# Kernel tuning notes

Hardware: AMD Instinct MI355X
Metric: run time of the kernel (lower is better)

## Reference

```python
import jax, jax.numpy as jnp
import numpy as np

N_EMBD = 1024
N_HEADS = 16
HEAD_DIM = N_EMBD // N_HEADS


def setup_inputs() -> dict:
    key = jax.random.key(0)
    ks = jax.random.split(key, 6)
    s = 1.0 / np.sqrt(N_EMBD)
    x = jax.random.normal(ks[0], (2, 2048, N_EMBD), dtype=jnp.float32)
    # torch Linear weights are [out, in]; y = x @ W.T
    Wk = jax.random.uniform(ks[1], (N_EMBD, N_EMBD), jnp.float32, -s, s)
    Wq = jax.random.uniform(ks[2], (N_EMBD, N_EMBD), jnp.float32, -s, s)
    Wv = jax.random.uniform(ks[3], (N_EMBD, N_EMBD), jnp.float32, -s, s)
    Wp = jax.random.uniform(ks[4], (N_EMBD, N_EMBD), jnp.float32, -s, s)
    bp = jax.random.uniform(ks[5], (N_EMBD,), jnp.float32, -s, s)
    return {"x": x, "Wq": Wq, "Wk": Wk, "Wv": Wv, "Wp": Wp, "bp": bp}


def reference(x, Wq, Wk, Wv, Wp, bp):
    B, T, C = x.shape
    H, D = N_HEADS, HEAD_DIM
    # projections (torch Linear: x @ W.T), reshape to [B, H, T, D]
    q = (x @ Wq.T).reshape(B, T, H, D).transpose(0, 2, 1, 3)
    k = (x @ Wk.T).reshape(B, T, H, D).transpose(0, 2, 1, 3)
    v = (x @ Wv.T).reshape(B, T, H, D).transpose(0, 2, 1, 3)
    # scaled causal attention, full [B,H,T,T] scores (faithful to original)
    att = jnp.einsum('bhqd,bhkd->bhqk', q, k) * (D ** -0.5)
    causal = jnp.tril(jnp.ones((T, T), dtype=bool))
    att = jnp.where(causal[None, None], att, -jnp.inf)
    att = jax.nn.softmax(att, axis=-1)
    out = jnp.einsum('bhqk,bhkd->bhqd', att, v)
    out = out.transpose(0, 2, 1, 3).reshape(B, T, C)
    return out @ Wp.T + bp
```

## Files before the change

kernel.cpp:

```cpp
#include <hip/hip_runtime.h>

typedef __bf16 bf16;
typedef __bf16 bf16x8 __attribute__((ext_vector_type(8)));
typedef float f32x4 __attribute__((ext_vector_type(4)));

#define DEV __device__ __forceinline__
#define NEG_BIG (-1.0e30f)


DEV bf16x8 load8(const bf16* p) { bf16x8 v; __builtin_memcpy(&v, p, 16); return v; }
DEV void store8(bf16* p, bf16x8 v) { __builtin_memcpy(p, &v, 16); }

DEV int sniff_bf16(const unsigned short* __restrict__ xr) {
  const int lane = threadIdx.x & 63;
  const unsigned short w = xr[lane * 2];
  const int e = (w >> 7) & 0xFF;
  const bool sane = ((w & 0x7FFF) == 0) || (e >= 97 && e <= 157);
  return __popcll(__ballot(sane)) >= 48;
}

DEV size_t frag_off(int row, int k) {
  const int rt = row >> 7, ks = k >> 6;
  const int chunk = (((row >> 4) & 7) * 2 + ((k >> 5) & 1)) * 64 + ((k >> 3) & 3) * 16 + (row & 15);
  return ((((size_t)rt * 16 + (size_t)ks) * 1024 + (size_t)chunk) << 3) | (size_t)(k & 7);
}

struct ConvArgs {
  const void* src[6];
  bf16* dst[6];
};

DEV bf16x8 cvt_load(const void* s, size_t e, int isbf) {
  bf16x8 v;
  if (isbf) v = load8((const bf16*)s + e);
  else {
    float tmp[8];
    __builtin_memcpy(tmp, (const float*)s + e, 32);
#pragma unroll
    for (int j = 0; j < 8; ++j) v[j] = (bf16)tmp[j];
  }
  return v;
}

__global__ __launch_bounds__(256) void convert_kernel(ConvArgs a) {
  const int isbf = sniff_bf16((const unsigned short*)a.src[0]);
  const int L = blockIdx.x;
  const int t = threadIdx.x;
  if (L == 1024) {
    if (t < 128) store8(a.dst[5] + t * 8, cvt_load(a.src[5], (size_t)t * 8, isbf));
    return;
  }
  int sel, tile;
  if (L < 512) { sel = 0; tile = L; }
  else         { sel = 1 + ((L - 512) >> 7); tile = (L - 512) & 127; }
  const int rt = tile >> 4, ks = tile & 15;
  const void* s = a.src[sel];
  bf16* d = a.dst[sel];

  __shared__ alignas(16) bf16 lds[128 * 9 * 8];
#pragma unroll
  for (int q = 0; q < 4; ++q) {
    const int lin = q * 256 + t;
    const int row = lin >> 3, k8 = lin & 7;
    const size_t se = (((size_t)(rt * 128 + row)) << 10) + (size_t)(ks * 64 + k8 * 8);
    store8(lds + (row * 9 + k8) * 8, cvt_load(s, se, isbf));
  }
  __syncthreads();
#pragma unroll
  for (int q = 0; q < 4; ++q) {
    const int c = q * 256 + t;
    const int row = ((c >> 7) & 7) * 16 + (c & 15);
    const int k8 = ((c >> 6) & 1) * 4 + ((c >> 4) & 3);
    store8(d + ((((size_t)tile << 10) + (size_t)c) << 3), load8(lds + (row * 9 + k8) * 8));
  }
}

DEV void gemm_reg_128(const bf16* __restrict__ A, const bf16* __restrict__ W,
                      int mblk, int nblk, f32x4 (&acc)[4][4]) {
  const int lane = threadIdx.x & 63, wid = threadIdx.x >> 6;
  const int wm = (wid >> 1) << 6, wn = (wid & 1) << 6;
  const int lr = lane & 15, lg = lane >> 4;
  const int arow = mblk * 128 + wm + lr;
  const int brow = nblk * 128 + wn + lr;

  const f32x4 zero = {0.f, 0.f, 0.f, 0.f};
#pragma unroll
  for (int i = 0; i < 4; ++i)
#pragma unroll
    for (int j = 0; j < 4; ++j) acc[i][j] = zero;

  for (int ks = 0; ks < 16; ++ks) {
    bf16x8 af[2][4], bf[2][4];
#pragma unroll
    for (int kh = 0; kh < 2; ++kh) {
      const int k = ks * 64 + kh * 32 + lg * 8;
#pragma unroll
      for (int i = 0; i < 4; ++i) af[kh][i] = load8(A + frag_off(arow + i * 16, k));
#pragma unroll
      for (int j = 0; j < 4; ++j) bf[kh][j] = load8(W + frag_off(brow + j * 16, k));
    }
#pragma unroll
    for (int kh = 0; kh < 2; ++kh)
#pragma unroll
      for (int i = 0; i < 4; ++i)
#pragma unroll
        for (int j = 0; j < 4; ++j)
          acc[i][j] = __builtin_amdgcn_mfma_f32_16x16x32_bf16(af[kh][i], bf[kh][j], acc[i][j], 0, 0, 0);
  }
}

DEV size_t frag_idx(int row, int col) {
  return ((size_t)(((col >> 5) * 4 + ((row >> 4) & 3)) * 64 + ((col >> 3) & 3) * 16 + (row & 15)) << 3)
         | (size_t)(col & 7);
}

__global__ __launch_bounds__(256, 3) void qkv_proj_kernel(
    const bf16* __restrict__ x, const bf16* __restrict__ Wq,
    const bf16* __restrict__ Wk, const bf16* __restrict__ Wv,
    bf16* __restrict__ q_ws, bf16* __restrict__ k_ws, bf16* __restrict__ vt_ws) {
  const int L = blockIdx.x;
  const int xcd = L & 7;
  const int idx = L >> 3;
  const int mblk = (xcd & 3) * 8 + (idx & 7);
  const int nm = (xcd >> 2) * 12 + (idx >> 3);
  const int nblk = nm & 7;
  const int mode = nm >> 3;
  const bf16* W = (mode == 0) ? Wq : (mode == 1) ? Wk : Wv;
  f32x4 acc[4][4];
  gemm_reg_128(x, W, mblk, nblk, acc);

  const int lane = threadIdx.x & 63, wid = threadIdx.x >> 6;
  const int wm = (wid >> 1) << 6, wn = (wid & 1) << 6;
  const int lr = lane & 15, lg = lane >> 4;
  const int m0 = mblk << 7, n0 = nblk << 7;
  const float vscale = (mode == 0) ? 0.125f : 1.0f;
  bf16* out = (mode == 0) ? q_ws : (mode == 1) ? k_ws : vt_ws;
#pragma unroll
  for (int i = 0; i < 4; ++i) {
#pragma unroll
    for (int r = 0; r < 4; ++r) {
      const int m = m0 + wm + i * 16 + lg * 4 + r;
      const int b = m >> 11, t = m & 2047;
#pragma unroll
      for (int j = 0; j < 4; ++j) {
        const int n = n0 + wn + j * 16 + lr;
        const int h = n >> 6, d = n & 63;
        const float v = acc[i][j][r] * vscale;
        const size_t base = ((size_t)(b * 16 + h) << 17) + ((size_t)(t >> 6) << 12);
        const size_t idx2 = base + ((mode < 2) ? frag_idx(t & 63, d) : frag_idx(d, t & 63));
        out[idx2] = (bf16)v;
      }
    }
  }
}

__global__ __launch_bounds__(128, 1) void attn_kernel(
    const bf16* __restrict__ q_ws, const bf16* __restrict__ k_ws,
    const bf16* __restrict__ vt_ws, bf16* __restrict__ a_ws) {
  const int L = blockIdx.x;
  const int xcd = L & 7;
  const int bh = xcd * 4 + ((L >> 3) & 3);
  const int p = L >> 5;
  const int tid = threadIdx.x;
  const int lane = tid & 63, w = tid >> 6;
  const int lr = lane & 15, lg = lane >> 4;
  const int fo = lg * 16 + lr;

  __shared__ alignas(16) bf16 Ps[2][32 * 72];
  bf16* ps = &Ps[w][0];

  const size_t hb = (size_t)bh << 17;
  const int b = bh >> 4, h = bh & 15;
  const f32x4 zero = {0.f, 0.f, 0.f, 0.f};

  for (int ph = 0; ph < 2; ++ph) {
    const int s = ph ? (63 - (p * 2 + w)) : (p * 2 + w);
    const int kmax = s >> 1;
    const size_t qtb = hb + ((size_t)(s >> 1) << 12);

    bf16x8 aq[2][2];
#pragma unroll
    for (int g = 0; g < 2; ++g) {
      const int rg = (s & 1) * 2 + g;
#pragma unroll
      for (int c2 = 0; c2 < 2; ++c2)
        aq[g][c2] = load8(q_ws + qtb + (size_t)(((c2 * 4 + rg) * 64 + fo) << 3));
    }

    f32x4 o_acc[2][4];
#pragma unroll
    for (int g = 0; g < 2; ++g)
#pragma unroll
      for (int j = 0; j < 4; ++j) o_acc[g][j] = zero;
    float lsum[2][4] = {{0.f, 0.f, 0.f, 0.f}, {0.f, 0.f, 0.f, 0.f}};

    auto load_k = [&](bf16x8 (&bk)[4][2], int kt) {
      const size_t ktb = hb + ((size_t)kt << 12);
#pragma unroll
      for (int j = 0; j < 4; ++j)
#pragma unroll
        for (int c2 = 0; c2 < 2; ++c2)
          bk[j][c2] = load8(k_ws + ktb + (size_t)(((c2 * 4 + j) * 64 + fo) << 3));
    };

    auto step = [&](const bf16x8 (&bk)[4][2], int kt, bool diag) {
      const size_t ktb = hb + ((size_t)kt << 12);
      bf16x8 bv[4][2];
#pragma unroll
      for (int j = 0; j < 4; ++j)
#pragma unroll
        for (int c2 = 0; c2 < 2; ++c2)
          bv[j][c2] = load8(vt_ws + ktb + (size_t)(((c2 * 4 + j) * 64 + fo) << 3));

      f32x4 sc[2][4];
#pragma unroll
      for (int g = 0; g < 2; ++g)
#pragma unroll
        for (int j = 0; j < 4; ++j) {
          sc[g][j] = __builtin_amdgcn_mfma_f32_16x16x32_bf16(aq[g][0], bk[j][0], zero, 0, 0, 0);
          sc[g][j] = __builtin_amdgcn_mfma_f32_16x16x32_bf16(aq[g][1], bk[j][1], sc[g][j], 0, 0, 0);
        }
      float pp[2][4][4];
#pragma unroll
      for (int g = 0; g < 2; ++g) {
#pragma unroll
        for (int j = 0; j < 4; ++j) {
#pragma unroll
          for (int r = 0; r < 4; ++r) {
            float v = sc[g][j][r];
            if (diag) {
              const int trow = s * 32 + g * 16 + lg * 4 + r;
              const int tcol = kt * 64 + j * 16 + lr;
              if (tcol > trow) v = NEG_BIG;
            }
            pp[g][j][r] = __expf(v);
          }
        }
#pragma unroll
        for (int r = 0; r < 4; ++r)
          lsum[g][r] += (pp[g][0][r] + pp[g][1][r]) + (pp[g][2][r] + pp[g][3][r]);
      }
#pragma unroll
      for (int g = 0; g < 2; ++g)
#pragma unroll
        for (int j = 0; j < 4; ++j)
#pragma unroll
          for (int r = 0; r < 4; ++r)
            ps[(g * 16 + lg * 4 + r) * 72 + j * 16 + lr] = (bf16)pp[g][j][r];
#pragma unroll
      for (int c2 = 0; c2 < 2; ++c2) {
#pragma unroll
        for (int g = 0; g < 2; ++g) {
          const bf16x8 ap = load8(ps + (g * 16 + lr) * 72 + c2 * 32 + lg * 8);
#pragma unroll
          for (int j = 0; j < 4; ++j)
            o_acc[g][j] = __builtin_amdgcn_mfma_f32_16x16x32_bf16(ap, bv[j][c2], o_acc[g][j], 0, 0, 0);
        }
      }
    };

    bf16x8 bkA[4][2], bkB[4][2];
    load_k(bkA, 0);
    int kt = 0;
    while (true) {
      if (kt < kmax) load_k(bkB, kt + 1);
      step(bkA, kt, kt == kmax);
      if (kt >= kmax) break;
      ++kt;
      if (kt < kmax) load_k(bkA, kt + 1);
      step(bkB, kt, kt == kmax);
      if (kt >= kmax) break;
      ++kt;
    }

#pragma unroll
    for (int g = 0; g < 2; ++g) {
#pragma unroll
      for (int r = 0; r < 4; ++r) {
        float v = lsum[g][r];
#pragma unroll
        for (int off = 1; off < 16; off <<= 1) v += __shfl_xor(v, off, 64);
        const float inv = 1.f / v;
        const int mrow = b * 2048 + s * 32 + g * 16 + lg * 4 + r;
#pragma unroll
        for (int j = 0; j < 4; ++j) {
          const int col = h * 64 + j * 16 + lr;
          a_ws[frag_off(mrow, col)] = (bf16)(o_acc[g][j][r] * inv);
        }
      }
    }
  }
}

__global__ __launch_bounds__(256, 3) void out_proj_kernel(
    const bf16* __restrict__ A, const bf16* __restrict__ Wp,
    const bf16* __restrict__ bp, void* __restrict__ out,
    const unsigned short* __restrict__ xraw) {
  const int L = blockIdx.x;
  const int xcd = L & 7;
  const int i2 = L >> 3;
  const int mblk = xcd * 4 + (i2 & 3);
  const int nblk = i2 >> 2;
  f32x4 acc[4][4];
  gemm_reg_128(A, Wp, mblk, nblk, acc);

  const int lane = threadIdx.x & 63, wid = threadIdx.x >> 6;
  const int wm = (wid >> 1) << 6, wn = (wid & 1) << 6;
  const int lr = lane & 15, lg = lane >> 4;
  const int m0 = mblk << 7, n0 = nblk << 7;
  const int isbf = sniff_bf16(xraw);
#pragma unroll
  for (int i = 0; i < 4; ++i) {
#pragma unroll
    for (int r = 0; r < 4; ++r) {
      const int m = m0 + wm + i * 16 + lg * 4 + r;
#pragma unroll
      for (int j = 0; j < 4; ++j) {
        const int n = n0 + wn + j * 16 + lr;
        const float v = acc[i][j][r] + (float)bp[n];
        const size_t idx = ((size_t)m << 10) | (size_t)n;
        if (isbf) ((bf16*)out)[idx] = (bf16)v;
        else      ((float*)out)[idx] = v;
      }
    }
  }
}

extern "C" void kernel_launch(void* const* d_in, const int* in_sizes, int n_in,
                              void* d_out, int out_size, void* d_ws, size_t ws_size,
                              hipStream_t stream) {
  (void)in_sizes; (void)n_in; (void)out_size;
  if (ws_size < (50u << 20)) return;

  char* ws = (char*)d_ws;
  bf16* q_ws  = (bf16*)(ws);
  bf16* k_ws  = (bf16*)(ws + (8u << 20));
  bf16* vt_ws = (bf16*)(ws + (16u << 20));
  bf16* a_ws  = (bf16*)(ws + (24u << 20));
  bf16* xc    = (bf16*)(ws + (32u << 20));
  bf16* Wqc   = (bf16*)(ws + (40u << 20));
  bf16* Wkc   = (bf16*)(ws + (42u << 20));
  bf16* Wvc   = (bf16*)(ws + (44u << 20));
  bf16* Wpc   = (bf16*)(ws + (46u << 20));
  bf16* bpc   = (bf16*)(ws + (48u << 20));

  ConvArgs ca;
  ca.src[0] = d_in[0]; ca.dst[0] = xc;
  ca.src[1] = d_in[1]; ca.dst[1] = Wqc;
  ca.src[2] = d_in[2]; ca.dst[2] = Wkc;
  ca.src[3] = d_in[3]; ca.dst[3] = Wvc;
  ca.src[4] = d_in[4]; ca.dst[4] = Wpc;
  ca.src[5] = d_in[5]; ca.dst[5] = bpc;
  convert_kernel<<<1025, 256, 0, stream>>>(ca);

  qkv_proj_kernel<<<768, 256, 0, stream>>>(xc, Wqc, Wkc, Wvc, q_ws, k_ws, vt_ws);
  attn_kernel<<<512, 128, 0, stream>>>(q_ws, k_ws, vt_ws, a_ws);
  out_proj_kernel<<<256, 256, 0, stream>>>(a_ws, Wpc, bpc, d_out,
                                           (const unsigned short*)d_in[0]);
}
```

Measured before the change: 209.0 us.

## Split attention into single-wave blocks per query strip and halve out-proj tiles

The attention kernel now runs one 64-thread wave per 32-row query strip, giving 2048 blocks instead of 512 blocks that each processed two strips over two phases. Strips are launched in longest-first order, and the diagonal key tile is processed first. The output projection switches to a direct-load 128x64 tile GEMM with 512 blocks instead of 128x128 tiles. The aim is better load balance and occupancy across CUs, in exchange for less operand reuse per block and more global loads.

```diff
diff --git a/kernel.cpp b/kernel.cpp
--- a/kernel.cpp
+++ b/kernel.cpp
@@ -154,139 +154,136 @@
   }
 }
 
-__global__ __launch_bounds__(128, 1) void attn_kernel(
+__global__ __launch_bounds__(64, 2) void attn_kernel(
     const bf16* __restrict__ q_ws, const bf16* __restrict__ k_ws,
     const bf16* __restrict__ vt_ws, bf16* __restrict__ a_ws) {
   const int L = blockIdx.x;
   const int xcd = L & 7;
-  const int bh = xcd * 4 + ((L >> 3) & 3);
-  const int p = L >> 5;
-  const int tid = threadIdx.x;
-  const int lane = tid & 63, w = tid >> 6;
+  const int idx = L >> 3;
+  const int bh = xcd * 4 + (idx & 3);
+  const int s = 63 - (idx >> 2);
+  const int qt = s >> 1;
+  const int rh = s & 1;
+  const int lane = threadIdx.x & 63;
   const int lr = lane & 15, lg = lane >> 4;
   const int fo = lg * 16 + lr;
 
-  __shared__ alignas(16) bf16 Ps[2][32 * 72];
-  bf16* ps = &Ps[w][0];
+  __shared__ alignas(16) bf16 Ps[32 * 72];
 
   const size_t hb = (size_t)bh << 17;
   const int b = bh >> 4, h = bh & 15;
   const f32x4 zero = {0.f, 0.f, 0.f, 0.f};
-
-  for (int ph = 0; ph < 2; ++ph) {
-    const int s = ph ? (63 - (p * 2 + w)) : (p * 2 + w);
-    const int kmax = s >> 1;
-    const size_t qtb = hb + ((size_t)(s >> 1) << 12);
-
-    bf16x8 aq[2][2];
+  const size_t qtb = hb + ((size_t)qt << 12);
+
+  bf16x8 aq[2][2];
+#pragma unroll
+  for (int g = 0; g < 2; ++g) {
+    const int rg = rh * 2 + g;
+#pragma unroll
+    for (int c2 = 0; c2 < 2; ++c2)
+      aq[g][c2] = load8(q_ws + qtb + (size_t)(((c2 * 4 + rg) * 64 + fo) << 3));
+  }
+
+  f32x4 o_acc[2][4];
+#pragma unroll
+  for (int g = 0; g < 2; ++g)
+#pragma unroll
+    for (int j = 0; j < 4; ++j) o_acc[g][j] = zero;
+  float lsum[2][4] = {{0.f, 0.f, 0.f, 0.f}, {0.f, 0.f, 0.f, 0.f}};
+
+  auto load_k = [&](bf16x8 (&bk)[4][2], int kt) {
+    const size_t ktb = hb + ((size_t)kt << 12);
+#pragma unroll
+    for (int j = 0; j < 4; ++j)
+#pragma unroll
+      for (int c2 = 0; c2 < 2; ++c2)
+        bk[j][c2] = load8(k_ws + ktb + (size_t)(((c2 * 4 + j) * 64 + fo) << 3));
+  };
+
+  auto step = [&](const bf16x8 (&bk)[4][2], int kt, bool diag) {
+    const size_t ktb = hb + ((size_t)kt << 12);
+    bf16x8 bv[4][2];
+#pragma unroll
+    for (int j = 0; j < 4; ++j)
+#pragma unroll
+      for (int c2 = 0; c2 < 2; ++c2)
+        bv[j][c2] = load8(vt_ws + ktb + (size_t)(((c2 * 4 + j) * 64 + fo) << 3));
+
+    f32x4 sc[2][4];
+#pragma unroll
+    for (int g = 0; g < 2; ++g)
+#pragma unroll
+      for (int j = 0; j < 4; ++j) {
+        sc[g][j] = __builtin_amdgcn_mfma_f32_16x16x32_bf16(aq[g][0], bk[j][0], zero, 0, 0, 0);
+        sc[g][j] = __builtin_amdgcn_mfma_f32_16x16x32_bf16(aq[g][1], bk[j][1], sc[g][j], 0, 0, 0);
+      }
+    float pp[2][4][4];
 #pragma unroll
     for (int g = 0; g < 2; ++g) {
-      const int rg = (s & 1) * 2 + g;
-#pragma unroll
-      for (int c2 = 0; c2 < 2; ++c2)
-        aq[g][c2] = load8(q_ws + qtb + (size_t)(((c2 * 4 + rg) * 64 + fo) << 3));
-    }
-
-    f32x4 o_acc[2][4];
+#pragma unroll
+      for (int j = 0; j < 4; ++j) {
+#pragma unroll
+        for (int r = 0; r < 4; ++r) {
+          float v = sc[g][j][r];
+          if (diag) {
+            const int row = s * 32 + g * 16 + lg * 4 + r;
+            const int col = kt * 64 + j * 16 + lr;
+            if (col > row) v = NEG_BIG;
+          }
+          pp[g][j][r] = __expf(v);
+        }
+      }
+#pragma unroll
+      for (int r = 0; r < 4; ++r)
+        lsum[g][r] += (pp[g][0][r] + pp[g][1][r]) + (pp[g][2][r] + pp[g][3][r]);
+    }
 #pragma unroll
     for (int g = 0; g < 2; ++g)
 #pragma unroll
-      for (int j = 0; j < 4; ++j) o_acc[g][j] = zero;
-    float lsum[2][4] = {{0.f, 0.f, 0.f, 0.f}, {0.f, 0.f, 0.f, 0.f}};
-
-    auto load_k = [&](bf16x8 (&bk)[4][2], int kt) {
-      const size_t ktb = hb + ((size_t)kt << 12);
-#pragma unroll
       for (int j = 0; j < 4; ++j)
 #pragma unroll
-        for (int c2 = 0; c2 < 2; ++c2)
-          bk[j][c2] = load8(k_ws + ktb + (size_t)(((c2 * 4 + j) * 64 + fo) << 3));
-    };
-
-    auto step = [&](const bf16x8 (&bk)[4][2], int kt, bool diag) {
-      const size_t ktb = hb + ((size_t)kt << 12);
-      bf16x8 bv[4][2];
-#pragma unroll
-      for (int j = 0; j < 4; ++j)
-#pragma unroll
-        for (int c2 = 0; c2 < 2; ++c2)
-          bv[j][c2] = load8(vt_ws + ktb + (size_t)(((c2 * 4 + j) * 64 + fo) << 3));
-
-      f32x4 sc[2][4];
-#pragma unroll
-      for (int g = 0; g < 2; ++g)
-#pragma unroll
-        for (int j = 0; j < 4; ++j) {
-          sc[g][j] = __builtin_amdgcn_mfma_f32_16x16x32_bf16(aq[g][0], bk[j][0], zero, 0, 0, 0);
-          sc[g][j] = __builtin_amdgcn_mfma_f32_16x16x32_bf16(aq[g][1], bk[j][1], sc[g][j], 0, 0, 0);
-        }
-      float pp[2][4][4];
+        for (int r = 0; r < 4; ++r)
+          Ps[(g * 16 + lg * 4 + r) * 72 + j * 16 + lr] = (bf16)pp[g][j][r];
+#pragma unroll
+    for (int c2 = 0; c2 < 2; ++c2) {
 #pragma unroll
       for (int g = 0; g < 2; ++g) {
-#pragma unroll
-        for (int j = 0; j < 4; ++j) {
-#pragma unroll
-          for (int r = 0; r < 4; ++r) {
-            float v = sc[g][j][r];
-            if (diag) {
-              const int trow = s * 32 + g * 16 + lg * 4 + r;
-              const int tcol = kt * 64 + j * 16 + lr;
-              if (tcol > trow) v = NEG_BIG;
-            }
-            pp[g][j][r] = __expf(v);
-          }
-        }
-#pragma unroll
-        for (int r = 0; r < 4; ++r)
-          lsum[g][r] += (pp[g][0][r] + pp[g][1][r]) + (pp[g][2][r] + pp[g][3][r]);
-      }
-#pragma unroll
-      for (int g = 0; g < 2; ++g)
+        const bf16x8 ap = load8(Ps + (g * 16 + lr) * 72 + c2 * 32 + lg * 8);
 #pragma unroll
         for (int j = 0; j < 4; ++j)
-#pragma unroll
-          for (int r = 0; r < 4; ++r)
-            ps[(g * 16 + lg * 4 + r) * 72 + j * 16 + lr] = (bf16)pp[g][j][r];
-#pragma unroll
-      for (int c2 = 0; c2 < 2; ++c2) {
-#pragma unroll
-        for (int g = 0; g < 2; ++g) {
-          const bf16x8 ap = load8(ps + (g * 16 + lr) * 72 + c2 * 32 + lg * 8);
-#pragma unroll
-          for (int j = 0; j < 4; ++j)
-            o_acc[g][j] = __builtin_amdgcn_mfma_f32_16x16x32_bf16(ap, bv[j][c2], o_acc[g][j], 0, 0, 0);
-        }
-      }
-    };
-
-    bf16x8 bkA[4][2], bkB[4][2];
-    load_k(bkA, 0);
-    int kt = 0;
-    while (true) {
-      if (kt < kmax) load_k(bkB, kt + 1);
-      step(bkA, kt, kt == kmax);
-      if (kt >= kmax) break;
-      ++kt;
-      if (kt < kmax) load_k(bkA, kt + 1);
-      step(bkB, kt, kt == kmax);
-      if (kt >= kmax) break;
-      ++kt;
-    }
-
-#pragma unroll
-    for (int g = 0; g < 2; ++g) {
-#pragma unroll
-      for (int r = 0; r < 4; ++r) {
-        float v = lsum[g][r];
-#pragma unroll
-        for (int off = 1; off < 16; off <<= 1) v += __shfl_xor(v, off, 64);
-        const float inv = 1.f / v;
-        const int mrow = b * 2048 + s * 32 + g * 16 + lg * 4 + r;
-#pragma unroll
-        for (int j = 0; j < 4; ++j) {
-          const int col = h * 64 + j * 16 + lr;
-          a_ws[frag_off(mrow, col)] = (bf16)(o_acc[g][j][r] * inv);
-        }
+          o_acc[g][j] = __builtin_amdgcn_mfma_f32_16x16x32_bf16(ap, bv[j][c2], o_acc[g][j], 0, 0, 0);
+      }
+    }
+  };
+
+  bf16x8 bkA[4][2], bkB[4][2];
+  const int n = qt;
+  load_k(bkA, qt);
+  if (n > 0) load_k(bkB, 0);
+  step(bkA, qt, true);
+  int kt = 0;
+  while (kt + 1 < n) {
+    load_k(bkA, kt + 1);
+    step(bkB, kt, false);
+    if (kt + 2 < n) load_k(bkB, kt + 2);
+    step(bkA, kt + 1, false);
+    kt += 2;
+  }
+  if (kt < n) step(bkB, kt, false);
+
+#pragma unroll
+  for (int g = 0; g < 2; ++g) {
+#pragma unroll
+    for (int r = 0; r < 4; ++r) {
+      float v = lsum[g][r];
+#pragma unroll
+      for (int off = 1; off < 16; off <<= 1) v += __shfl_xor(v, off, 64);
+      const float inv = 1.f / v;
+      const int mrow = b * 2048 + s * 32 + g * 16 + lg * 4 + r;
+#pragma unroll
+      for (int j = 0; j < 4; ++j) {
+        const int col = h * 64 + j * 16 + lr;
+        a_ws[frag_off(mrow, col)] = (bf16)(o_acc[g][j][r] * inv);
       }
     }
   }
@@ -300,14 +297,40 @@
   const int xcd = L & 7;
   const int i2 = L >> 3;
   const int mblk = xcd * 4 + (i2 & 3);
-  const int nblk = i2 >> 2;
-  f32x4 acc[4][4];
-  gemm_reg_128(A, Wp, mblk, nblk, acc);
-
+  const int n64 = i2 >> 2;
   const int lane = threadIdx.x & 63, wid = threadIdx.x >> 6;
-  const int wm = (wid >> 1) << 6, wn = (wid & 1) << 6;
+  const int wm = (wid >> 1) << 6, wn = (wid & 1) << 5;
   const int lr = lane & 15, lg = lane >> 4;
-  const int m0 = mblk << 7, n0 = nblk << 7;
+  const int arow = mblk * 128 + wm + lr;
+  const int brow = n64 * 64 + wn + lr;
+
+  const f32x4 zero = {0.f, 0.f, 0.f, 0.f};
+  f32x4 acc[4][2];
+#pragma unroll
+  for (int i = 0; i < 4; ++i)
+#pragma unroll
+    for (int j = 0; j < 2; ++j) acc[i][j] = zero;
+
+  for (int ks = 0; ks < 16; ++ks) {
+    bf16x8 af[2][4], bf[2][2];
+#pragma unroll
+    for (int kh = 0; kh < 2; ++kh) {
+      const int k = ks * 64 + kh * 32 + lg * 8;
+#pragma unroll
+      for (int i = 0; i < 4; ++i) af[kh][i] = load8(A + frag_off(arow + i * 16, k));
+#pragma unroll
+      for (int j = 0; j < 2; ++j) bf[kh][j] = load8(Wp + frag_off(brow + j * 16, k));
+    }
+#pragma unroll
+    for (int kh = 0; kh < 2; ++kh)
+#pragma unroll
+      for (int i = 0; i < 4; ++i)
+#pragma unroll
+        for (int j = 0; j < 2; ++j)
+          acc[i][j] = __builtin_amdgcn_mfma_f32_16x16x32_bf16(af[kh][i], bf[kh][j], acc[i][j], 0, 0, 0);
+  }
+
+  const int m0 = mblk << 7;
   const int isbf = sniff_bf16(xraw);
 #pragma unroll
   for (int i = 0; i < 4; ++i) {
@@ -315,8 +338,8 @@
     for (int r = 0; r < 4; ++r) {
       const int m = m0 + wm + i * 16 + lg * 4 + r;
 #pragma unroll
-      for (int j = 0; j < 4; ++j) {
-        const int n = n0 + wn + j * 16 + lr;
+      for (int j = 0; j < 2; ++j) {
+        const int n = n64 * 64 + wn + j * 16 + lr;
         const float v = acc[i][j][r] + (float)bp[n];
         const size_t idx = ((size_t)m << 10) | (size_t)n;
         if (isbf) ((bf16*)out)[idx] = (bf16)v;
@@ -354,7 +377,7 @@
   convert_kernel<<<1025, 256, 0, stream>>>(ca);
 
   qkv_proj_kernel<<<768, 256, 0, stream>>>(xc, Wqc, Wkc, Wvc, q_ws, k_ws, vt_ws);
-  attn_kernel<<<512, 128, 0, stream>>>(q_ws, k_ws, vt_ws, a_ws);
-  out_proj_kernel<<<256, 256, 0, stream>>>(a_ws, Wpc, bpc, d_out,
+  attn_kernel<<<2048, 64, 0, stream>>>(q_ws, k_ws, vt_ws, a_ws);
+  out_proj_kernel<<<512, 256, 0, stream>>>(a_ws, Wpc, bpc, d_out,
                                            (const unsigned short*)d_in[0]);
 }
```

Result: faster. 190.2 us (-9.0%).
